# Kernel optimization log

Measured on AMD Instinct MI355X. Metric: run time of the kernel, lower is better.

The kernel has to match this reference:

```python
import jax, jax.numpy as jnp
import numpy as np
import math


def _favor(X, W, is_query):
    # X: [B,L,H,M], W: [M,M] (shared across batch, matching tf.repeat of a single QR matrix)
    M = X.shape[-1]
    dn = 1.0 / math.sqrt(math.sqrt(M))
    X = dn * X
    diag = (jnp.sum(X * X, axis=-1) * (0.5 * dn * dn))[..., None]  # [B,L,H,1]
    dot = jnp.einsum('dm,blhm->blhd', W, X)                         # [B,L,H,M]
    if is_query:
        mx = jnp.max(X, axis=-1, keepdims=True)
    else:
        mx = jnp.max(X, axis=(1, 3), keepdims=True)  # axes (-3,-1) = (L, M)
    return (1.0 / math.sqrt(M)) * jnp.exp(dot - diag - mx + 1e-8)


def _causal_attn(qs, ks, vs):
    # qs,ks: [B,L,H,M]; vs: [B,L,H,D]. Cumulative KV-state recurrence via lax.scan.
    B, L, H, M = ks.shape
    D = vs.shape[-1]

    def step(carry, x):
        sums, snorm = carry          # [B,H,M,D], [B,H,M]
        q, k, v = x                  # [B,H,M], [B,H,M], [B,H,D]
        snorm = snorm + k
        sums = sums + k[..., :, None] * v[..., None, :]
        num = jnp.einsum('bhmd,bhm->bhd', sums, q)
        den = jnp.sum(q * snorm, axis=-1, keepdims=True)
        return (sums, snorm), num / den

    init = (jnp.zeros((B, H, M, D), qs.dtype), jnp.zeros((B, H, M), qs.dtype))
    xs = (jnp.swapaxes(qs, 0, 1), jnp.swapaxes(ks, 0, 1), jnp.swapaxes(vs, 0, 1))
    _, out = jax.lax.scan(step, init, xs)   # out: [L,B,H,D]
    return jnp.swapaxes(out, 0, 1)          # [B,L,H,D]


def _make_favor_proj(rng, M):
    # Mirrors: W ~ N(0,1); Q,_ = qr(W); Q /= norm(Q, axis=-1) (TF broadcast divides columns); Q *= sqrt(M)
    W = rng.standard_normal((M, M)).astype(np.float32)
    Q, _ = np.linalg.qr(W)
    n = np.linalg.norm(Q, axis=1)          # row norms, shape (M,)
    Q = Q / n[None, :]                     # TF broadcasting quirk: divide column j by n[j]
    return jnp.asarray(Q * math.sqrt(M), dtype=jnp.float32)


def setup_inputs() -> dict:
    B, L, d_model, H = 2, 4096, 1024, 16
    M = d_model // H
    key = jax.random.key(0)
    k1, k2, k3 = jax.random.split(key, 3)
    rng = np.random.default_rng(0)

    def dense_w(dout):
        return jnp.asarray(rng.standard_normal((d_model, dout)).astype(np.float32) * 0.02)

    return {
        'queries': jax.random.normal(k1, (B, L, d_model), jnp.float32),
        'keys': jax.random.normal(k2, (B, L, d_model), jnp.float32),
        'values': jax.random.normal(k3, (B, L, d_model), jnp.float32),
        'Wq': dense_w(H * M), 'bq': jnp.zeros((H * M,), jnp.float32),
        'Wk': dense_w(H * M), 'bk': jnp.zeros((H * M,), jnp.float32),
        'Wv': dense_w(H * M), 'bv': jnp.zeros((H * M,), jnp.float32),
        'Wo': dense_w(d_model), 'bo': jnp.zeros((d_model,), jnp.float32),
        'Wfq': _make_favor_proj(rng, M),
        'Wfk': _make_favor_proj(rng, M),
        'H': H,
    }


def reference(queries, keys, values, Wq, bq, Wk, bk, Wv, bv, Wo, bo, Wfq, Wfk, H):
    N, L, _ = queries.shape
    S = keys.shape[1]
    q = (queries @ Wq + bq).reshape(N, L, H, -1)
    k = (keys @ Wk + bk).reshape(N, S, H, -1)
    v = (values @ Wv + bv).reshape(N, S, H, -1)
    Ql = _favor(q, Wfq, is_query=True)
    Kl = _favor(k, Wfk, is_query=False)
    V = _causal_attn(Ql, Kl, v)             # [N,L,H,D]
    return V.reshape(N, L, -1) @ Wo + bo    # [N,L,d_model]
```

## Files before the change

### kernel.cpp

```cpp
#include <hip/hip_runtime.h>
#include <math.h>

#define BATCH 2
#define SEQ   4096
#define DM    1024
#define NH    16
#define MD    64
#define NROW  (BATCH*SEQ)
#define RQ    (BATCH*SEQ*NH)
#define NCHUNK 64
#define CT     64
#define DN    0.35355339059327373f
#define INV_SQRT_M 0.125f
#define PITCH 72
#define STSZ  (65*64)
#define DIAG_SCALE (0.125f * 0.0625f)

typedef unsigned short ushort_t;
typedef short bf8_t __attribute__((ext_vector_type(8)));
typedef float f4_t  __attribute__((ext_vector_type(4)));
typedef ushort_t us8_t __attribute__((ext_vector_type(8)));

__device__ static inline ushort_t f2bf(float f) {
    union { float f; unsigned u; } v; v.f = f;
    unsigned r = v.u + 0x7FFFu + ((v.u >> 16) & 1u);
    return (ushort_t)(r >> 16);
}
__device__ static inline float bf2f(ushort_t u) {
    union { unsigned u; float f; } v; v.u = ((unsigned)u) << 16;
    return v.f;
}

__device__ static inline void async_ld16(const ushort_t* g, ushort_t* l) {
    __builtin_amdgcn_global_load_lds(
        (const __attribute__((address_space(1))) unsigned int*)g,
        (__attribute__((address_space(3))) unsigned int*)l,
        16, 0, 0);
}

__device__ static inline void swizzle_mn(int lid, int* bm, int* bn) {
    *bm = (((lid & 7) << 3) + (lid >> 6)) << 7;
    *bn = ((lid >> 3) & 7) << 7;
}

__global__ __launch_bounds__(256) void prep_weights(
    const float* __restrict__ W0, const float* __restrict__ W1,
    const float* __restrict__ W2, const float* __restrict__ W3,
    ushort_t* __restrict__ WT, unsigned* __restrict__ kmOrd)
{
    if (blockIdx.z == 0 && blockIdx.x == 0 && blockIdx.y == 0 && threadIdx.x < 32)
        kmOrd[threadIdx.x] = 0u;
    const float* W = blockIdx.z == 0 ? W0 : (blockIdx.z == 1 ? W1 : (blockIdx.z == 2 ? W2 : W3));
    ushort_t* dst = WT + (size_t)blockIdx.z * DM * DM;
    __shared__ float t[32][33];
    const int k0 = blockIdx.x * 32, n0 = blockIdx.y * 32;
    const int tx = threadIdx.x & 31, ty = threadIdx.x >> 5;
    #pragma unroll
    for (int r = 0; r < 32; r += 8)
        t[ty + r][tx] = W[(size_t)(k0 + ty + r) * 1024 + n0 + tx];
    __syncthreads();
    #pragma unroll
    for (int r = 0; r < 32; r += 8)
        dst[(size_t)(n0 + ty + r) * 1024 + k0 + tx] = f2bf(t[tx][ty + r]);
}

__global__ __launch_bounds__(256) void cvt_qkv(
    const float* __restrict__ Q, const float* __restrict__ K,
    const float* __restrict__ V, ushort_t* __restrict__ Y)
{
    const int y = blockIdx.y;
    const float* X = y == 0 ? Q : (y == 1 ? K : V);
    ushort_t* dst = Y + (size_t)y * NROW * DM;
    int i = blockIdx.x * 256 + threadIdx.x;
    const float4* X4 = (const float4*)X;
    float4 a = X4[i * 2], b = X4[i * 2 + 1];
    us8_t o;
    o[0]=f2bf(a.x); o[1]=f2bf(a.y); o[2]=f2bf(a.z); o[3]=f2bf(a.w);
    o[4]=f2bf(b.x); o[5]=f2bf(b.y); o[6]=f2bf(b.z); o[7]=f2bf(b.w);
    *(us8_t*)&dst[i * 8] = o;
}

__device__ static inline void gemm_core(
    const ushort_t* __restrict__ A, const ushort_t* __restrict__ BT,
    ushort_t* As, ushort_t* Bs, int bm, int bn, int tid, f4_t acc[4][4])
{
    const int lane = tid & 63;
    const int wm = ((tid >> 6) >> 1) * 64, wn = ((tid >> 6) & 1) * 64;
    const int quad = lane >> 4, l15 = lane & 15;
    const int srow = tid >> 3, sch = tid & 7;
    const ushort_t* gA = A  + (size_t)(bm + srow) * DM + sch * 8;
    const ushort_t* gB = BT + (size_t)(bn + srow) * DM + sch * 8;
    ushort_t* lA = &As[srow * 64 + sch * 8];
    ushort_t* lB = &Bs[srow * 64 + sch * 8];

    for (int k0 = 0; k0 < DM; k0 += 64) {
        __syncthreads();
        #pragma unroll
        for (int c = 0; c < 4; ++c) {
            async_ld16(gA + (size_t)c * 32 * DM + k0, lA + c * 32 * 64);
            async_ld16(gB + (size_t)c * 32 * DM + k0, lB + c * 32 * 64);
        }
        __syncthreads();
        #pragma unroll
        for (int ks = 0; ks < 2; ++ks) {
            bf8_t af[4], bfr[4];
            #pragma unroll
            for (int i = 0; i < 4; ++i) {
                af[i]  = *(const bf8_t*)&As[(wm + i * 16 + l15) * 64 + ks * 32 + quad * 8];
                bfr[i] = *(const bf8_t*)&Bs[(wn + i * 16 + l15) * 64 + ks * 32 + quad * 8];
            }
            #pragma unroll
            for (int i = 0; i < 4; ++i)
                #pragma unroll
                for (int j = 0; j < 4; ++j)
                    acc[i][j] = __builtin_amdgcn_mfma_f32_16x16x32_bf16(
                        af[i], bfr[j], acc[i][j], 0, 0, 0);
        }
    }
}

__global__ __launch_bounds__(256) void gemm_qkv(
    const ushort_t* __restrict__ Xc, const ushort_t* __restrict__ WT,
    const float* __restrict__ bq, const float* __restrict__ bk,
    const float* __restrict__ bv, ushort_t* __restrict__ Obase,
    unsigned* __restrict__ kmOrd)
{
    __shared__ ushort_t As[128 * 64];
    __shared__ ushort_t Bs[128 * 64];
    const int z = blockIdx.z;
    const ushort_t* A  = Xc + (size_t)z * NROW * DM;
    const ushort_t* BT = WT + (size_t)z * DM * DM;
    const float* bias = z == 0 ? bq : (z == 1 ? bk : bv);
    ushort_t* Cbf = Obase + (size_t)z * NROW * DM;

    const int tid = threadIdx.x;
    int bm, bn;
    swizzle_mn(blockIdx.x + (blockIdx.y << 3), &bm, &bn);
    const int lane = tid & 63;
    const int wm = ((tid >> 6) >> 1) * 64, wn = ((tid >> 6) & 1) * 64;
    const int quad = lane >> 4, l15 = lane & 15;

    f4_t acc[4][4] = {};
    gemm_core(A, BT, As, Bs, bm, bn, tid, acc);

    float mx = -3.4e38f;
    #pragma unroll
    for (int j = 0; j < 4; ++j) {
        const int col = bn + wn + j * 16 + l15;
        const float bb = bias[col];
        #pragma unroll
        for (int i = 0; i < 4; ++i) {
            const int row0 = bm + wm + i * 16 + quad * 4;
            #pragma unroll
            for (int r = 0; r < 4; ++r) {
                float v = acc[i][j][r] + bb;
                mx = fmaxf(mx, v);
                Cbf[(size_t)(row0 + r) * DM + col] = f2bf(v);
            }
        }
    }
    if (z == 1) {
        #pragma unroll
        for (int off = 32; off; off >>= 1) mx = fmaxf(mx, __shfl_xor(mx, off));
        if (lane == 0) {
            const int b = bm >> 12;
            const int h = (bn + wn) >> 6;
            unsigned ub = __float_as_uint(mx);
            unsigned enc = (ub & 0x80000000u) ? ~ub : (ub | 0x80000000u);
            atomicMax(&kmOrd[b * NH + h], enc);
        }
    }
}

__global__ __launch_bounds__(256) void gemm_out(
    const ushort_t* __restrict__ A, const ushort_t* __restrict__ BT,
    const float* __restrict__ bias, float* __restrict__ C)
{
    __shared__ ushort_t As[128 * 64];
    __shared__ ushort_t Bs[128 * 64];
    const int tid = threadIdx.x;
    int bm, bn;
    swizzle_mn(blockIdx.x + (blockIdx.y << 3), &bm, &bn);
    const int lane = tid & 63;
    const int wm = ((tid >> 6) >> 1) * 64, wn = ((tid >> 6) & 1) * 64;
    const int quad = lane >> 4, l15 = lane & 15;

    f4_t acc[4][4] = {};
    gemm_core(A, BT, As, Bs, bm, bn, tid, acc);

    #pragma unroll
    for (int j = 0; j < 4; ++j) {
        const int col = bn + wn + j * 16 + l15;
        const float bb = bias[col];
        #pragma unroll
        for (int i = 0; i < 4; ++i) {
            const int row0 = bm + wm + i * 16 + quad * 4;
            #pragma unroll
            for (int r = 0; r < 4; ++r)
                C[(size_t)(row0 + r) * DM + col] = acc[i][j][r] + bb;
        }
    }
}

__global__ __launch_bounds__(256) void favor_k_mfma(
    ushort_t* __restrict__ X, const float* __restrict__ Wf,
    const unsigned* __restrict__ kmOrd)
{
    __shared__ ushort_t Xs[64 * PITCH];
    __shared__ ushort_t Ws[64 * PITCH];
    __shared__ float ssp[64][4];
    __shared__ float diag[64], mxr[64];
    const int tid = threadIdx.x;
    const int lane = tid & 63, w = tid >> 6;
    const int quad = lane >> 4, l15 = lane & 15;
    const int rbase = blockIdx.x * 64;

    #pragma unroll
    for (int r = 0; r < 2; ++r) {
        int idx = tid + r * 256;
        int row = idx >> 3, ch = idx & 7;
        *(us8_t*)&Xs[row * PITCH + ch * 8] =
            *(const us8_t*)&X[(size_t)(rbase + row) * 64 + ch * 8];
    }
    const float4* Wf4 = (const float4*)Wf;
    #pragma unroll
    for (int i = 0; i < 4; ++i) {
        int f4i = tid + i * 256;
        int row = f4i >> 4, q4 = f4i & 15;
        float4 wv = Wf4[f4i];
        Ws[row * PITCH + q4 * 4 + 0] = f2bf(DN * wv.x);
        Ws[row * PITCH + q4 * 4 + 1] = f2bf(DN * wv.y);
        Ws[row * PITCH + q4 * 4 + 2] = f2bf(DN * wv.z);
        Ws[row * PITCH + q4 * 4 + 3] = f2bf(DN * wv.w);
    }
    __syncthreads();

    {
        const int row = tid >> 2, seg = tid & 3;
        const us8_t* xp = (const us8_t*)&Xs[row * PITCH + seg * 16];
        us8_t a = xp[0], b2 = xp[1];
        float ss = 0.f;
        #pragma unroll
        for (int j = 0; j < 8; ++j) {
            float x0 = bf2f(a[j]), x1 = bf2f(b2[j]);
            ss += x0 * x0 + x1 * x1;
        }
        ssp[row][seg] = ss;
    }
    __syncthreads();
    if (tid < 64) {
        diag[tid] = (ssp[tid][0] + ssp[tid][1] + ssp[tid][2] + ssp[tid][3]) * DIAG_SCALE;
        int rg = rbase + tid;
        int h = rg & (NH - 1);
        int b = rg >> 16;
        unsigned u = kmOrd[b * NH + h];
        unsigned bits = (u & 0x80000000u) ? (u & 0x7FFFFFFFu) : ~u;
        mxr[tid] = DN * __uint_as_float(bits);
    }
    __syncthreads();

    bf8_t xf[2];
    #pragma unroll
    for (int ks = 0; ks < 2; ++ks)
        xf[ks] = *(const bf8_t*)&Xs[(w * 16 + l15) * PITCH + ks * 32 + quad * 8];
    f4_t acc[4] = {};
    #pragma unroll
    for (int dt = 0; dt < 4; ++dt)
        #pragma unroll
        for (int ks = 0; ks < 2; ++ks) {
            bf8_t wfr = *(const bf8_t*)&Ws[(dt * 16 + l15) * PITCH + ks * 32 + quad * 8];
            acc[dt] = __builtin_amdgcn_mfma_f32_16x16x32_bf16(xf[ks], wfr, acc[dt], 0, 0, 0);
        }
    __syncthreads();

    #pragma unroll
    for (int r = 0; r < 4; ++r) {
        int row = w * 16 + quad * 4 + r;
        float d_ = diag[row], m_ = mxr[row];
        #pragma unroll
        for (int dt = 0; dt < 4; ++dt) {
            float e = acc[dt][r] - d_ - m_ + 1e-8f;
            X[(size_t)(rbase + row) * 64 + dt * 16 + l15] = f2bf(INV_SQRT_M * expf(e));
        }
    }
}

__global__ __launch_bounds__(256) void chunk_sums_mfma(
    const ushort_t* __restrict__ Kbf, const ushort_t* __restrict__ Vbf,
    ushort_t* __restrict__ ST)
{
    const int bx = blockIdx.x;
    const int c = bx & 63, h = (bx >> 6) & 15, b = bx >> 10;
    __shared__ ushort_t Kt[64 * PITCH];
    __shared__ ushort_t Vt[80 * PITCH];
    const int tid = threadIdx.x;
    const int lane = tid & 63, w = tid >> 6;
    const int quad = lane >> 4, l15 = lane & 15;

    const size_t gbase = ((size_t)(b * SEQ + c * CT)) * DM + h * MD;
    #pragma unroll
    for (int r = 0; r < 2; ++r) {
        int ch = w + r * 4;
        int t = lane;
        us8_t kv = *(const us8_t*)&Kbf[gbase + (size_t)t * DM + ch * 8];
        us8_t vv = *(const us8_t*)&Vbf[gbase + (size_t)t * DM + ch * 8];
        #pragma unroll
        for (int j = 0; j < 8; ++j) {
            Kt[(ch * 8 + j) * PITCH + t] = kv[j];
            Vt[(ch * 8 + j) * PITCH + t] = vv[j];
        }
    }
    if (tid < 64) Vt[64 * PITCH + tid] = (ushort_t)0x3F80;
    __syncthreads();

    ushort_t* Sg = ST + (size_t)((b * NH + h) * NCHUNK + c) * STSZ;

    bf8_t vf[2];
    #pragma unroll
    for (int ks = 0; ks < 2; ++ks)
        vf[ks] = *(const bf8_t*)&Vt[(w * 16 + l15) * PITCH + ks * 32 + quad * 8];
    f4_t acc[4] = {};
    #pragma unroll
    for (int mt = 0; mt < 4; ++mt)
        #pragma unroll
        for (int ks = 0; ks < 2; ++ks) {
            bf8_t kf = *(const bf8_t*)&Kt[(mt * 16 + l15) * PITCH + ks * 32 + quad * 8];
            acc[mt] = __builtin_amdgcn_mfma_f32_16x16x32_bf16(vf[ks], kf, acc[mt], 0, 0, 0);
        }
    #pragma unroll
    for (int mt = 0; mt < 4; ++mt)
        #pragma unroll
        for (int r = 0; r < 4; ++r)
            Sg[(w * 16 + quad * 4 + r) * 64 + mt * 16 + l15] = f2bf(acc[mt][r]);

    if (w == 0) {
        bf8_t vf4[2];
        #pragma unroll
        for (int ks = 0; ks < 2; ++ks)
            vf4[ks] = *(const bf8_t*)&Vt[(64 + l15) * PITCH + ks * 32 + quad * 8];
        f4_t accz[4] = {};
        #pragma unroll
        for (int mt = 0; mt < 4; ++mt)
            #pragma unroll
            for (int ks = 0; ks < 2; ++ks) {
                bf8_t kf = *(const bf8_t*)&Kt[(mt * 16 + l15) * PITCH + ks * 32 + quad * 8];
                accz[mt] = __builtin_amdgcn_mfma_f32_16x16x32_bf16(vf4[ks], kf, accz[mt], 0, 0, 0);
            }
        if (quad == 0) {
            #pragma unroll
            for (int mt = 0; mt < 4; ++mt)
                Sg[64 * 64 + mt * 16 + l15] = f2bf(accz[mt][0]);
        }
    }
}

__global__ __launch_bounds__(256) void prefix_scan_st(ushort_t* __restrict__ ST)
{
    const int sb = blockIdx.x / 17;
    const int e = (blockIdx.x % 17) * 256 + threadIdx.x;
    if (e >= STSZ) return;
    ushort_t* p = ST + (size_t)sb * NCHUNK * STSZ + e;
    ushort_t v[NCHUNK];
    #pragma unroll
    for (int c = 0; c < NCHUNK; ++c) v[c] = p[(size_t)c * STSZ];
    float run = 0.f;
    #pragma unroll
    for (int c = 0; c < NCHUNK; ++c) {
        float cur = bf2f(v[c]);
        p[(size_t)c * STSZ] = f2bf(run);
        run += cur;
    }
}

__global__ __launch_bounds__(256) void intra_attn_mfma(
    const ushort_t* __restrict__ Qraw, const ushort_t* __restrict__ Kbf,
    const ushort_t* __restrict__ Vbf, const ushort_t* __restrict__ ST,
    const float* __restrict__ Wfq, ushort_t* __restrict__ Obf)
{
    const int bx = blockIdx.x;
    const int c = bx & 63, h = (bx >> 6) & 15, b = bx >> 10;
    __shared__ ushort_t Qs[64 * PITCH];
    __shared__ ushort_t Ks[64 * PITCH];
    __shared__ ushort_t Vt[80 * PITCH];
    __shared__ ushort_t St[80 * PITCH];
    __shared__ ushort_t Ws[64 * PITCH];
    __shared__ float ssp[64][4];
    __shared__ float mxp[64][4];
    __shared__ float diag[64], mxr[64], dens[64];
    const int tid = threadIdx.x;
    const int lane = tid & 63, w = tid >> 6;
    const int quad = lane >> 4, l15 = lane & 15;

    const size_t gbase = ((size_t)(b * SEQ + c * CT)) * DM + h * MD;

    #pragma unroll
    for (int r = 0; r < 2; ++r) {
        int idx = tid + r * 256;
        int row = idx >> 3, ch = idx & 7;
        us8_t qv = *(const us8_t*)&Qraw[gbase + (size_t)row * DM + ch * 8];
        us8_t kv = *(const us8_t*)&Kbf[gbase + (size_t)row * DM + ch * 8];
        *(us8_t*)&Qs[row * PITCH + ch * 8] = qv;
        *(us8_t*)&Ks[row * PITCH + ch * 8] = kv;
    }
    #pragma unroll
    for (int r = 0; r < 2; ++r) {
        int ch = w + r * 4;
        int t = lane;
        us8_t vv = *(const us8_t*)&Vbf[gbase + (size_t)t * DM + ch * 8];
        #pragma unroll
        for (int j = 0; j < 8; ++j) Vt[(ch * 8 + j) * PITCH + t] = vv[j];
    }
    #pragma unroll
    for (int r = 0; r < 4; ++r) {
        int idx = tid + r * 256;
        int row = 64 + (idx >> 6), t = idx & 63;
        Vt[row * PITCH + t] = (row == 64) ? (ushort_t)0x3F80 : (ushort_t)0;
    }
    const us8_t* Sg8 = (const us8_t*)(ST + (size_t)((b * NH + h) * NCHUNK + c) * STSZ);
    #pragma unroll
    for (int r = 0; r < 3; ++r) {
        int idx = tid + r * 256;
        if (idx < 520) {
            int d = idx >> 3, mo = (idx & 7) * 8;
            *(us8_t*)&St[d * PITCH + mo] = Sg8[idx];
        }
        int idx2 = idx - 520;
        if (idx2 >= 0 && idx2 < 120) {
            int row = 65 + (idx2 >> 3), mo = (idx2 & 7) * 8;
            us8_t z = {};
            *(us8_t*)&St[row * PITCH + mo] = z;
        }
    }
    const float4* Wf4 = (const float4*)Wfq;
    #pragma unroll
    for (int i = 0; i < 4; ++i) {
        int f4i = tid + i * 256;
        int row = f4i >> 4, q4 = f4i & 15;
        float4 wv = Wf4[f4i];
        Ws[row * PITCH + q4 * 4 + 0] = f2bf(DN * wv.x);
        Ws[row * PITCH + q4 * 4 + 1] = f2bf(DN * wv.y);
        Ws[row * PITCH + q4 * 4 + 2] = f2bf(DN * wv.z);
        Ws[row * PITCH + q4 * 4 + 3] = f2bf(DN * wv.w);
    }
    __syncthreads();

    {
        const int row = tid >> 2, seg = tid & 3;
        const us8_t* xp = (const us8_t*)&Qs[row * PITCH + seg * 16];
        us8_t a = xp[0], b2 = xp[1];
        float ss = 0.f, mx = -3.4e38f;
        #pragma unroll
        for (int j = 0; j < 8; ++j) {
            float x0 = bf2f(a[j]), x1 = bf2f(b2[j]);
            ss += x0 * x0 + x1 * x1;
            mx = fmaxf(mx, fmaxf(x0, x1));
        }
        ssp[row][seg] = ss;
        mxp[row][seg] = mx;
    }
    __syncthreads();
    if (tid < 64) {
        diag[tid] = (ssp[tid][0] + ssp[tid][1] + ssp[tid][2] + ssp[tid][3]) * DIAG_SCALE;
        mxr[tid] = DN * fmaxf(fmaxf(mxp[tid][0], mxp[tid][1]),
                              fmaxf(mxp[tid][2], mxp[tid][3]));
    }
    __syncthreads();

    {
        bf8_t xf[2];
        #pragma unroll
        for (int ks = 0; ks < 2; ++ks)
            xf[ks] = *(const bf8_t*)&Qs[(w * 16 + l15) * PITCH + ks * 32 + quad * 8];
        f4_t facc[4] = {};
        #pragma unroll
        for (int dt = 0; dt < 4; ++dt)
            #pragma unroll
            for (int ks = 0; ks < 2; ++ks) {
                bf8_t wfr = *(const bf8_t*)&Ws[(dt * 16 + l15) * PITCH + ks * 32 + quad * 8];
                facc[dt] = __builtin_amdgcn_mfma_f32_16x16x32_bf16(xf[ks], wfr, facc[dt], 0, 0, 0);
            }
        __syncthreads();
        #pragma unroll
        for (int r = 0; r < 4; ++r) {
            int row = w * 16 + quad * 4 + r;
            float d_ = diag[row], m_ = mxr[row];
            #pragma unroll
            for (int dt = 0; dt < 4; ++dt) {
                float e = facc[dt][r] - d_ - m_ + 1e-8f;
                Qs[row * PITCH + dt * 16 + l15] = f2bf(INV_SQRT_M * expf(e));
            }
        }
    }
    __syncthreads();

    bf8_t qf[2];
    #pragma unroll
    for (int ks = 0; ks < 2; ++ks)
        qf[ks] = *(const bf8_t*)&Qs[(w * 16 + l15) * PITCH + ks * 32 + quad * 8];
    f4_t accA[4] = {};
    #pragma unroll
    for (int jt = 0; jt < 4; ++jt)
        #pragma unroll
        for (int ks = 0; ks < 2; ++ks) {
            bf8_t kf = *(const bf8_t*)&Ks[(jt * 16 + l15) * PITCH + ks * 32 + quad * 8];
            accA[jt] = __builtin_amdgcn_mfma_f32_16x16x32_bf16(qf[ks], kf, accA[jt], 0, 0, 0);
        }
    __syncthreads();
    #pragma unroll
    for (int jt = 0; jt < 4; ++jt) {
        int j = jt * 16 + l15;
        #pragma unroll
        for (int r = 0; r < 4; ++r) {
            int i = w * 16 + quad * 4 + r;
            float a = (j <= i) ? accA[jt][r] : 0.f;
            Ks[i * PITCH + j] = f2bf(a);
        }
    }
    __syncthreads();

    bf8_t af[2];
    #pragma unroll
    for (int ks = 0; ks < 2; ++ks)
        af[ks] = *(const bf8_t*)&Ks[(w * 16 + l15) * PITCH + ks * 32 + quad * 8];
    f4_t acc[5] = {};
    #pragma unroll
    for (int dt = 0; dt < 5; ++dt)
        #pragma unroll
        for (int ks = 0; ks < 2; ++ks) {
            bf8_t sf = *(const bf8_t*)&St[(dt * 16 + l15) * PITCH + ks * 32 + quad * 8];
            acc[dt] = __builtin_amdgcn_mfma_f32_16x16x32_bf16(qf[ks], sf, acc[dt], 0, 0, 0);
            bf8_t vf = *(const bf8_t*)&Vt[(dt * 16 + l15) * PITCH + ks * 32 + quad * 8];
            acc[dt] = __builtin_amdgcn_mfma_f32_16x16x32_bf16(af[ks], vf, acc[dt], 0, 0, 0);
        }
    if (l15 == 0) {
        #pragma unroll
        for (int r = 0; r < 4; ++r) dens[w * 16 + quad * 4 + r] = acc[4][r];
    }
    __syncthreads();

    #pragma unroll
    for (int r = 0; r < 4; ++r) {
        int i = w * 16 + quad * 4 + r;
        float inv = 1.0f / dens[i];
        #pragma unroll
        for (int dt = 0; dt < 4; ++dt)
            Obf[gbase + (size_t)i * DM + dt * 16 + l15] = f2bf(acc[dt][r] * inv);
    }
}

extern "C" void kernel_launch(void* const* d_in, const int* in_sizes, int n_in,
                              void* d_out, int out_size, void* d_ws, size_t ws_size,
                              hipStream_t stream)
{
    const float* queries = (const float*)d_in[0];
    const float* keys    = (const float*)d_in[1];
    const float* values  = (const float*)d_in[2];
    const float* Wq = (const float*)d_in[3];  const float* bq = (const float*)d_in[4];
    const float* Wk = (const float*)d_in[5];  const float* bk = (const float*)d_in[6];
    const float* Wv = (const float*)d_in[7];  const float* bv = (const float*)d_in[8];
    const float* Wo = (const float*)d_in[9];  const float* bo = (const float*)d_in[10];
    const float* Wfq = (const float*)d_in[11];
    const float* Wfk = (const float*)d_in[12];

    char* ws = (char*)d_ws;
    unsigned* kmOrd = (unsigned*)ws;
    ushort_t* STb = (ushort_t*)(ws + 256);
    ushort_t* qbf = STb + (size_t)32 * NCHUNK * STSZ;
    ushort_t* kbf = qbf + (size_t)NROW * DM;
    ushort_t* vbf = kbf + (size_t)NROW * DM;
    ushort_t* obf = vbf + (size_t)NROW * DM;
    ushort_t* xcvt = obf + (size_t)NROW * DM;
    ushort_t* wT  = xcvt + (size_t)3 * NROW * DM;
    ushort_t* WoT = wT + (size_t)3 * DM * DM;

    prep_weights<<<dim3(32, 32, 4), 256, 0, stream>>>(Wq, Wk, Wv, Wo, wT, kmOrd);

    const int n8 = NROW * DM / 8;
    cvt_qkv<<<dim3(n8 / 256, 3), 256, 0, stream>>>(queries, keys, values, xcvt);

    gemm_qkv<<<dim3(8, 64, 3), 256, 0, stream>>>(xcvt, wT, bq, bk, bv, qbf, kmOrd);

    favor_k_mfma<<<RQ / 64, 256, 0, stream>>>(kbf, Wfk, kmOrd);

    chunk_sums_mfma<<<BATCH * NH * NCHUNK, 256, 0, stream>>>(kbf, vbf, STb);
    prefix_scan_st<<<32 * 17, 256, 0, stream>>>(STb);
    intra_attn_mfma<<<BATCH * NH * NCHUNK, 256, 0, stream>>>(qbf, kbf, vbf, STb, Wfq, obf);

    gemm_out<<<dim3(8, 64), 256, 0, stream>>>(obf, WoT, bo, (float*)d_out);
}
```

Before: 340.8 us.

## Use 256x256 double-buffered GEMM tiles with LDS swizzle for projections

Replaces the 128x128 single-buffered GEMM core with a 256x256 tile run by 512 threads (8 waves, 128x64 each). The K loop is double-buffered with explicit vmcnt waits, and LDS slots are XOR-swizzled to avoid bank conflicts. This targets low arithmetic intensity and load stalls in the QKV and output projections. The cost is more registers and LDS per block (64KB), and only 128 blocks per GEMM, which may underfill the CUs.

```diff
diff --git a/kernel.cpp b/kernel.cpp
--- a/kernel.cpp
+++ b/kernel.cpp
@@ -38,9 +38,96 @@
         16, 0, 0);
 }
 
-__device__ static inline void swizzle_mn(int lid, int* bm, int* bn) {
-    *bm = (((lid & 7) << 3) + (lid >> 6)) << 7;
-    *bn = ((lid >> 3) & 7) << 7;
+__device__ static inline void sbar() {
+    __builtin_amdgcn_sched_barrier(0);
+    __builtin_amdgcn_s_barrier();
+    __builtin_amdgcn_sched_barrier(0);
+}
+#define VMCNT(n) do { asm volatile("s_waitcnt vmcnt(" #n ")" ::: "memory"); \
+                      __builtin_amdgcn_sched_barrier(0); } while (0)
+
+#define BUFE (256*64)
+
+__device__ static inline void g256_compute(
+    const ushort_t* As, const ushort_t* Bs, int wr, int wc,
+    int quad, int l15, f4_t acc[8][4])
+{
+    #pragma unroll
+    for (int ks = 0; ks < 2; ++ks) {
+        bf8_t af[8], bfr[4];
+        const int slot = ((ks << 2) | quad) ^ (l15 & 7);
+        #pragma unroll
+        for (int i = 0; i < 8; ++i) {
+            const int row = wr * 128 + i * 16 + l15;
+            af[i] = *(const bf8_t*)&As[row * 64 + slot * 8];
+        }
+        #pragma unroll
+        for (int j = 0; j < 4; ++j) {
+            const int row = wc * 64 + j * 16 + l15;
+            bfr[j] = *(const bf8_t*)&Bs[row * 64 + slot * 8];
+        }
+        __builtin_amdgcn_s_setprio(1);
+        #pragma unroll
+        for (int i = 0; i < 8; ++i)
+            #pragma unroll
+            for (int j = 0; j < 4; ++j)
+                acc[i][j] = __builtin_amdgcn_mfma_f32_16x16x32_bf16(
+                    af[i], bfr[j], acc[i][j], 0, 0, 0);
+        __builtin_amdgcn_s_setprio(0);
+    }
+}
+
+__device__ static inline void gemm256_core(
+    const ushort_t* __restrict__ A, const ushort_t* __restrict__ BT,
+    ushort_t* As, ushort_t* Bs, int bm, int bn, int tid, f4_t acc[8][4])
+{
+    const int lane = tid & 63, w = tid >> 6;
+    const int wr = w >> 2, wc = w & 3;
+    const int quad = lane >> 4, l15 = lane & 15;
+    const int lrow = lane >> 3;
+    const int kslot = (lane & 7) ^ lrow;
+
+    auto stage = [&](int t, int sel) {
+        #pragma unroll
+        for (int c = 0; c < 4; ++c) {
+            const int r0 = w * 8 + c * 64;
+            const int r = r0 + lrow;
+            const ushort_t* ga = A  + (size_t)(bm + r) * DM + t * 64 + kslot * 8;
+            const ushort_t* gb = BT + (size_t)(bn + r) * DM + t * 64 + kslot * 8;
+            async_ld16(ga, &As[sel * BUFE + r0 * 64]);
+            async_ld16(gb, &Bs[sel * BUFE + r0 * 64]);
+        }
+    };
+
+    stage(0, 0);
+    stage(1, 1);
+    VMCNT(8);
+    sbar();
+
+    #pragma unroll 1
+    for (int tt = 0; tt < 7; ++tt) {
+        g256_compute(&As[0],    &Bs[0],    wr, wc, quad, l15, acc);
+        sbar();
+        stage(2 * tt + 2, 0);
+        VMCNT(8);
+        sbar();
+
+        g256_compute(&As[BUFE], &Bs[BUFE], wr, wc, quad, l15, acc);
+        sbar();
+        stage(2 * tt + 3, 1);
+        VMCNT(8);
+        sbar();
+    }
+    g256_compute(&As[0], &Bs[0], wr, wc, quad, l15, acc);
+    VMCNT(0);
+    sbar();
+    g256_compute(&As[BUFE], &Bs[BUFE], wr, wc, quad, l15, acc);
+}
+
+__device__ static inline void swz128(int bx, int* bm, int* bn) {
+    const int nid = (bx & 7) * 16 + (bx >> 3);
+    *bm = (nid >> 2) << 8;
+    *bn = (nid & 3) << 8;
 }
 
 __global__ __launch_bounds__(256) void prep_weights(
@@ -80,54 +167,15 @@
     *(us8_t*)&dst[i * 8] = o;
 }
 
-__device__ static inline void gemm_core(
-    const ushort_t* __restrict__ A, const ushort_t* __restrict__ BT,
-    ushort_t* As, ushort_t* Bs, int bm, int bn, int tid, f4_t acc[4][4])
-{
-    const int lane = tid & 63;
-    const int wm = ((tid >> 6) >> 1) * 64, wn = ((tid >> 6) & 1) * 64;
-    const int quad = lane >> 4, l15 = lane & 15;
-    const int srow = tid >> 3, sch = tid & 7;
-    const ushort_t* gA = A  + (size_t)(bm + srow) * DM + sch * 8;
-    const ushort_t* gB = BT + (size_t)(bn + srow) * DM + sch * 8;
-    ushort_t* lA = &As[srow * 64 + sch * 8];
-    ushort_t* lB = &Bs[srow * 64 + sch * 8];
-
-    for (int k0 = 0; k0 < DM; k0 += 64) {
-        __syncthreads();
-        #pragma unroll
-        for (int c = 0; c < 4; ++c) {
-            async_ld16(gA + (size_t)c * 32 * DM + k0, lA + c * 32 * 64);
-            async_ld16(gB + (size_t)c * 32 * DM + k0, lB + c * 32 * 64);
-        }
-        __syncthreads();
-        #pragma unroll
-        for (int ks = 0; ks < 2; ++ks) {
-            bf8_t af[4], bfr[4];
-            #pragma unroll
-            for (int i = 0; i < 4; ++i) {
-                af[i]  = *(const bf8_t*)&As[(wm + i * 16 + l15) * 64 + ks * 32 + quad * 8];
-                bfr[i] = *(const bf8_t*)&Bs[(wn + i * 16 + l15) * 64 + ks * 32 + quad * 8];
-            }
-            #pragma unroll
-            for (int i = 0; i < 4; ++i)
-                #pragma unroll
-                for (int j = 0; j < 4; ++j)
-                    acc[i][j] = __builtin_amdgcn_mfma_f32_16x16x32_bf16(
-                        af[i], bfr[j], acc[i][j], 0, 0, 0);
-        }
-    }
-}
-
-__global__ __launch_bounds__(256) void gemm_qkv(
+__global__ __launch_bounds__(512, 2) void gemm_qkv(
     const ushort_t* __restrict__ Xc, const ushort_t* __restrict__ WT,
     const float* __restrict__ bq, const float* __restrict__ bk,
     const float* __restrict__ bv, ushort_t* __restrict__ Obase,
     unsigned* __restrict__ kmOrd)
 {
-    __shared__ ushort_t As[128 * 64];
-    __shared__ ushort_t Bs[128 * 64];
-    const int z = blockIdx.z;
+    __shared__ ushort_t As[2 * BUFE];
+    __shared__ ushort_t Bs[2 * BUFE];
+    const int z = blockIdx.y;
     const ushort_t* A  = Xc + (size_t)z * NROW * DM;
     const ushort_t* BT = WT + (size_t)z * DM * DM;
     const float* bias = z == 0 ? bq : (z == 1 ? bk : bv);
@@ -135,22 +183,22 @@
 
     const int tid = threadIdx.x;
     int bm, bn;
-    swizzle_mn(blockIdx.x + (blockIdx.y << 3), &bm, &bn);
-    const int lane = tid & 63;
-    const int wm = ((tid >> 6) >> 1) * 64, wn = ((tid >> 6) & 1) * 64;
+    swz128(blockIdx.x, &bm, &bn);
+    const int lane = tid & 63, w = tid >> 6;
+    const int wr = w >> 2, wc = w & 3;
     const int quad = lane >> 4, l15 = lane & 15;
 
-    f4_t acc[4][4] = {};
-    gemm_core(A, BT, As, Bs, bm, bn, tid, acc);
+    f4_t acc[8][4] = {};
+    gemm256_core(A, BT, As, Bs, bm, bn, tid, acc);
 
     float mx = -3.4e38f;
     #pragma unroll
     for (int j = 0; j < 4; ++j) {
-        const int col = bn + wn + j * 16 + l15;
+        const int col = bn + wc * 64 + j * 16 + l15;
         const float bb = bias[col];
         #pragma unroll
-        for (int i = 0; i < 4; ++i) {
-            const int row0 = bm + wm + i * 16 + quad * 4;
+        for (int i = 0; i < 8; ++i) {
+            const int row0 = bm + wr * 128 + i * 16 + quad * 4;
             #pragma unroll
             for (int r = 0; r < 4; ++r) {
                 float v = acc[i][j][r] + bb;
@@ -164,7 +212,7 @@
         for (int off = 32; off; off >>= 1) mx = fmaxf(mx, __shfl_xor(mx, off));
         if (lane == 0) {
             const int b = bm >> 12;
-            const int h = (bn + wn) >> 6;
+            const int h = (bn + wc * 64) >> 6;
             unsigned ub = __float_as_uint(mx);
             unsigned enc = (ub & 0x80000000u) ? ~ub : (ub | 0x80000000u);
             atomicMax(&kmOrd[b * NH + h], enc);
@@ -172,29 +220,29 @@
     }
 }
 
-__global__ __launch_bounds__(256) void gemm_out(
+__global__ __launch_bounds__(512, 2) void gemm_out(
     const ushort_t* __restrict__ A, const ushort_t* __restrict__ BT,
     const float* __restrict__ bias, float* __restrict__ C)
 {
-    __shared__ ushort_t As[128 * 64];
-    __shared__ ushort_t Bs[128 * 64];
+    __shared__ ushort_t As[2 * BUFE];
+    __shared__ ushort_t Bs[2 * BUFE];
     const int tid = threadIdx.x;
     int bm, bn;
-    swizzle_mn(blockIdx.x + (blockIdx.y << 3), &bm, &bn);
-    const int lane = tid & 63;
-    const int wm = ((tid >> 6) >> 1) * 64, wn = ((tid >> 6) & 1) * 64;
+    swz128(blockIdx.x, &bm, &bn);
+    const int lane = tid & 63, w = tid >> 6;
+    const int wr = w >> 2, wc = w & 3;
     const int quad = lane >> 4, l15 = lane & 15;
 
-    f4_t acc[4][4] = {};
-    gemm_core(A, BT, As, Bs, bm, bn, tid, acc);
+    f4_t acc[8][4] = {};
+    gemm256_core(A, BT, As, Bs, bm, bn, tid, acc);
 
     #pragma unroll
     for (int j = 0; j < 4; ++j) {
-        const int col = bn + wn + j * 16 + l15;
+        const int col = bn + wc * 64 + j * 16 + l15;
         const float bb = bias[col];
         #pragma unroll
-        for (int i = 0; i < 4; ++i) {
-            const int row0 = bm + wm + i * 16 + quad * 4;
+        for (int i = 0; i < 8; ++i) {
+            const int row0 = bm + wr * 128 + i * 16 + quad * 4;
             #pragma unroll
             for (int r = 0; r < 4; ++r)
                 C[(size_t)(row0 + r) * DM + col] = acc[i][j][r] + bb;
@@ -578,7 +626,7 @@
     const int n8 = NROW * DM / 8;
     cvt_qkv<<<dim3(n8 / 256, 3), 256, 0, stream>>>(queries, keys, values, xcvt);
 
-    gemm_qkv<<<dim3(8, 64, 3), 256, 0, stream>>>(xcvt, wT, bq, bk, bv, qbf, kmOrd);
+    gemm_qkv<<<dim3(128, 3), 512, 0, stream>>>(xcvt, wT, bq, bk, bv, qbf, kmOrd);
 
     favor_k_mfma<<<RQ / 64, 256, 0, stream>>>(kbf, Wfk, kmOrd);
 
@@ -586,5 +634,5 @@
     prefix_scan_st<<<32 * 17, 256, 0, stream>>>(STb);
     intra_attn_mfma<<<BATCH * NH * NCHUNK, 256, 0, stream>>>(qbf, kbf, vbf, STb, Wfq, obf);
 
-    gemm_out<<<dim3(8, 64), 256, 0, stream>>>(obf, WoT, bo, (float*)d_out);
-}
+    gemm_out<<<128, 512, 0, stream>>>(obf, WoT, bo, (float*)d_out);
+}
```

Measured after the change: 339.9 us. About the same (-0.3%).
